# Kernel optimization log

Measured on AMD Instinct MI355X. Metric: run time of the kernel, lower is better.

## Reference

```python
import jax, jax.numpy as jnp
import numpy as np

B, IN_DIM, H, OUT_DIM, T = 2048, 1024, 2048, 1024, 10


def setup_inputs() -> dict:
    key = jax.random.key(0)
    ks = jax.random.split(key, 16)
    s = lambda d: 1.0 / np.sqrt(d)
    inp = {
        "x": jax.random.normal(ks[0], (B, IN_DIM), jnp.float32),
        "z0": jax.random.normal(ks[1], (B, H), jnp.float32),
        "noise": jax.random.normal(ks[2], (T, B, H), jnp.float32),
        # input_embed: Linear(IN,H) -> SiLU -> Linear(H,H)
        "w1_in": jax.random.normal(ks[3], (IN_DIM, H), jnp.float32) * s(IN_DIM),
        "b1_in": jnp.zeros((H,), jnp.float32),
        "w2_in": jax.random.normal(ks[4], (H, H), jnp.float32) * s(H),
        "b2_in": jnp.zeros((H,), jnp.float32),
        # T blocks: Linear(2H,H) -> SiLU -> Linear(H,H), stacked over T
        "wA": jax.random.normal(ks[5], (T, 2 * H, H), jnp.float32) * s(2 * H),
        "bA": jnp.zeros((T, H), jnp.float32),
        "wB": jax.random.normal(ks[6], (T, H, H), jnp.float32) * s(H),
        "bB": jnp.zeros((T, H), jnp.float32),
        # classifier Linear(H, OUT)
        "wC": jax.random.normal(ks[7], (H, OUT_DIM), jnp.float32) * s(H),
        "bC": jnp.zeros((OUT_DIM,), jnp.float32),
    }
    return inp


def _forward(x, z0, noise, w1_in, b1_in, w2_in, b2_in, wA, bA, wB, bB, wC, bC):
    # input embedding
    h = jax.nn.silu(x @ w1_in + b1_in)
    x_embed = h @ w2_in + b2_in  # (B, H)

    alpha = jnp.linspace(0.99, 0.9, T).astype(x.dtype)          # (T,)
    noise_scale = jnp.sqrt(1.0 - alpha)                          # (T,)

    def step(z, per_t):
        wA_t, bA_t, wB_t, bB_t, n_t, a_t, ns_t = per_t
        u = jax.nn.silu(jnp.concatenate([z, x_embed], axis=-1) @ wA_t + bA_t)
        u = u @ wB_t + bB_t
        z_next = a_t * u + (1.0 - a_t) * z + ns_t * n_t
        return z_next, None

    z_final, _ = jax.lax.scan(step, z0, (wA, bA, wB, bB, noise, alpha, noise_scale))
    return z_final @ wC + bC  # (B, OUT_DIM)


def reference(x, z0, noise, w1_in, b1_in, w2_in, b2_in, wA, bA, wB, bB, wC, bC):
    return _forward(x, z0, noise, w1_in, b1_in, w2_in, b2_in, wA, bA, wB, bB, wC, bC)
```

## Files before the change

### kernel.cpp

```cpp
#include <hip/hip_runtime.h>
#include <math.h>

typedef _Float16 f16;
typedef _Float16 f16x4 __attribute__((ext_vector_type(4)));
typedef _Float16 f16x8 __attribute__((ext_vector_type(8)));
typedef float f32x4 __attribute__((ext_vector_type(4)));
typedef float fvec4 __attribute__((ext_vector_type(4)));

#define EP_SILU 0
#define EP_LIN  1
#define EP_ZUP  2
#define EP_OUT  3
#define EP_ADDP 4

struct TDesc {
  const float* W;
  f16* WT;
  long long sW, sWT;
  int R, C, nMat;
};

__device__ __forceinline__ void gll16(const void* g, void* l) {
  __builtin_amdgcn_global_load_lds((__attribute__((address_space(1))) void*)g,
                                   (__attribute__((address_space(3))) void*)l,
                                   16, 0, 0);
}

__device__ __forceinline__ void stage_tile(const f16* __restrict__ g, int ld,
                                           f16* ldsTile, int tid, int wid) {
#pragma unroll
  for (int p = 0; p < 2; ++p) {
    int row = p * 64 + (tid >> 2);
    int col = (tid & 3) * 8;
    gll16(g + (size_t)row * ld + col, ldsTile + p * 2048 + wid * 512);
  }
}

__device__ __forceinline__ void stage8s(const f16* __restrict__ g, int ld,
                                        f16* ldsTile, int tid) {
  int row = tid >> 2;
  int q = (tid & 3) ^ ((tid >> 3) & 3);
  gll16(g + (size_t)row * ld + q * 8, ldsTile + tid * 8);
}

__device__ __forceinline__ void tpose_tile(const float* __restrict__ W,
                                           f16* __restrict__ WT, int R, int C,
                                           int r0, int c0, f16 (*t)[72],
                                           int tid) {
#pragma unroll
  for (int p = 0; p < 2; ++p) {
    int lin = p * 2048 + tid * 4;
    int r = lin >> 6, c4 = lin & 63;
    fvec4 v = *(const fvec4*)(W + (size_t)(r0 + r) * C + c0 + c4);
    t[c4 + 0][r] = (f16)v[0];
    t[c4 + 1][r] = (f16)v[1];
    t[c4 + 2][r] = (f16)v[2];
    t[c4 + 3][r] = (f16)v[3];
  }
  __syncthreads();
#pragma unroll
  for (int p = 0; p < 2; ++p) {
    int lin = p * 2048 + tid * 4;
    int c = lin >> 6, r4 = lin & 63;
    f16x4 h;
    h[0] = t[c][r4 + 0];
    h[1] = t[c][r4 + 1];
    h[2] = t[c][r4 + 2];
    h[3] = t[c][r4 + 3];
    *(f16x4*)(WT + (size_t)(c0 + c) * R + r0 + r4) = h;
  }
  __syncthreads();
}

__device__ void run_role(const TDesc d, int rid, int nr, f16 (*t)[72],
                         int tid) {
  if (d.nMat <= 0 || d.W == nullptr) return;
  int tR = d.R >> 6, tC = d.C >> 6;
  int tpm = tR * tC, tot = tpm * d.nMat;
  for (int i = rid; i < tot; i += nr) {
    int m = i / tpm, rem = i - m * tpm;
    int r0 = (rem % tR) << 6, c0 = (rem / tR) << 6;
    tpose_tile(d.W + (size_t)m * d.sW, d.WT + (size_t)m * d.sWT, d.R, d.C, r0,
               c0, t, tid);
  }
}

#define GEMM64_ITER(KP, VM, DO_STAGE)                                         \
  {                                                                           \
    asm volatile("s_waitcnt vmcnt(" #VM ")" ::: "memory");                    \
    __builtin_amdgcn_s_barrier();                                             \
    const int slot_ = (KP) & 1;                                               \
    const f16* LA_ = base + slot_ * 12288 + h * 2048;                         \
    const f16* LB_ = base + slot_ * 12288 + 4096 + h * 4096;                  \
    f16x8 a_[2], b_[4];                                                       \
    _Pragma("unroll") for (int m_ = 0; m_ < 2; ++m_) a_[m_] =                 \
        *(const f16x8*)(LA_ +                                                 \
                        ((wr * 32 + m_ * 16 + lr) * 32 + (kg ^ xq) * 8));     \
    _Pragma("unroll") for (int n_ = 0; n_ < 4; ++n_) b_[n_] =                 \
        *(const f16x8*)(LB_ +                                                 \
                        ((wc * 64 + n_ * 16 + lr) * 32 + (kg ^ xq) * 8));     \
    asm volatile("s_waitcnt lgkmcnt(0)" ::: "memory");                        \
    __builtin_amdgcn_s_barrier();                                             \
    if (DO_STAGE) stageAB((KP) + 2, slot_);                                   \
    _Pragma("unroll") for (int m_ = 0; m_ < 2; ++m_)                          \
        _Pragma("unroll") for (int n_ = 0; n_ < 4; ++n_) acc[m_][n_] =        \
            __builtin_amdgcn_mfma_f32_16x16x32_f16(a_[m_], b_[n_],            \
                                                   acc[m_][n_], 0, 0, 0);     \
  }

template <int EP>
__global__ void __launch_bounds__(512)
gemm64(const f16* __restrict__ A, int lda, const f16* __restrict__ BT,
       int ldb, int K, int N, int gx, int nbGemm,
       const float* __restrict__ bias, const f16* __restrict__ addP,
       f16* __restrict__ outH, float* __restrict__ outF,
       const f16* __restrict__ zOld, const float* __restrict__ noise,
       float aT, float nsT, TDesc dA, TDesc dB) {
  __shared__ __align__(16) char smem[49152];
  const int tid = threadIdx.x;
  const int bid = blockIdx.x;

  if (bid >= nbGemm) {
    int rid = bid - nbGemm, nr = (int)gridDim.x - nbGemm;
    f16(*t)[72] = reinterpret_cast<f16(*)[72]>(smem);
    run_role(dA, rid, nr, t, tid);
    run_role(dB, rid, nr, t, tid);
    return;
  }

  const int cpx = nbGemm >> 3;
  const int swz = (bid & 7) * cpx + (bid >> 3);
  const int by = swz / gx, bx = swz % gx;
  const int m0 = by * 64, n0 = bx * 128;

  const int lane = tid & 63, wid = tid >> 6;
  const int q = wid & 3, h = wid >> 2;
  const int wr = q >> 1, wc = q & 1;
  const int lr = lane & 15, kg = lane >> 4;
  const int xq = (lr >> 1) & 3;

  f16* base = (f16*)smem;
  f32x4 acc[2][4] = {};

  const int nkp = K >> 6;
  auto stageAB = [&](int kp, int slot) {
    int k0 = kp << 6;
    f16* s = base + slot * 12288;
    {
      int half = tid >> 8;
      int pos = tid & 255;
      int row = pos >> 2;
      int qq = (pos & 3) ^ ((pos >> 3) & 3);
      gll16(A + (size_t)(m0 + row) * lda + k0 + half * 32 + qq * 8,
            s + half * 2048 + pos * 8);
    }
    stage8s(BT + (size_t)n0 * ldb + k0, ldb, s + 4096, tid);
    stage8s(BT + (size_t)n0 * ldb + k0 + 32, ldb, s + 8192, tid);
  };

  stageAB(0, 0);
  stageAB(1, 1);
  int kp = 0;
  for (; kp < nkp - 1; ++kp) GEMM64_ITER(kp, 3, (kp + 2 < nkp));
  GEMM64_ITER(kp, 0, 0);

  float* red = (float*)smem;
  if (h == 1) {
#pragma unroll
    for (int m = 0; m < 2; ++m)
#pragma unroll
      for (int n = 0; n < 4; ++n) {
        int row = wr * 32 + m * 16 + kg * 4;
        int col = wc * 64 + n * 16 + lr;
        int rs = row ^ ((col & 7) << 2);
        *(f32x4*)&red[(size_t)col * 64 + rs] = acc[m][n];
      }
  }
  __syncthreads();
  if (h != 0) return;

  float bcol[4];
  if constexpr (EP != EP_ADDP) {
#pragma unroll
    for (int n = 0; n < 4; ++n) bcol[n] = bias[n0 + wc * 64 + n * 16 + lr];
  }

#pragma unroll
  for (int m = 0; m < 2; ++m) {
    int rowb = m0 + wr * 32 + m * 16 + kg * 4;
    int rowl = wr * 32 + m * 16 + kg * 4;
#pragma unroll
    for (int n = 0; n < 4; ++n) {
      int col = n0 + wc * 64 + n * 16 + lr;
      int coll = wc * 64 + n * 16 + lr;
      int rsl = rowl ^ ((coll & 7) << 2);
      f32x4 osum = acc[m][n] + *(const f32x4*)&red[(size_t)coll * 64 + rsl];
#pragma unroll
      for (int r = 0; r < 4; ++r) {
        size_t idx = (size_t)(rowb + r) * N + col;
        float v = osum[r];
        if constexpr (EP == EP_ADDP) v += (float)addP[idx];
        else v += bcol[n];
        if constexpr (EP == EP_SILU || EP == EP_ADDP) {
          v = v / (1.0f + __expf(-v));
          outH[idx] = (f16)v;
        } else if constexpr (EP == EP_LIN) {
          outH[idx] = (f16)v;
        } else if constexpr (EP == EP_OUT) {
          outF[idx] = v;
        } else {
          float zn = aT * v + (1.0f - aT) * (float)zOld[idx] + nsT * noise[idx];
          outH[idx] = (f16)zn;
        }
      }
    }
  }
}

#define GEMM8_ITER(KP, VM, DO_STAGE)                                          \
  {                                                                           \
    asm volatile("s_waitcnt vmcnt(" #VM ")" ::: "memory");                    \
    __builtin_amdgcn_s_barrier();                                             \
    const int slot_ = (KP) & 1;                                               \
    const f16* LA_ = base + slot_ * 16384 + h * 4096;                         \
    const f16* LB_ = base + slot_ * 16384 + 8192 + h * 4096;                  \
    f16x8 a_[4], b_[4];                                                       \
    _Pragma("unroll") for (int m_ = 0; m_ < 4; ++m_) a_[m_] =                 \
        *(const f16x8*)(LA_ +                                                 \
                        ((wr * 64 + m_ * 16 + lr) * 32 + (kg ^ xq) * 8));     \
    _Pragma("unroll") for (int n_ = 0; n_ < 4; ++n_) b_[n_] =                 \
        *(const f16x8*)(LB_ +                                                 \
                        ((wc * 64 + n_ * 16 + lr) * 32 + (kg ^ xq) * 8));     \
    asm volatile("s_waitcnt lgkmcnt(0)" ::: "memory");                        \
    __builtin_amdgcn_s_barrier();                                             \
    if (DO_STAGE) stageAB((KP) + 2, slot_);                                   \
    _Pragma("unroll") for (int m_ = 0; m_ < 4; ++m_)                          \
        _Pragma("unroll") for (int n_ = 0; n_ < 4; ++n_) acc[m_][n_] =        \
            __builtin_amdgcn_mfma_f32_16x16x32_f16(a_[m_], b_[n_],            \
                                                   acc[m_][n_], 0, 0, 0);     \
  }

template <int EP>
__global__ void __launch_bounds__(512)
gemm8(const f16* __restrict__ A, int lda, const f16* __restrict__ BT, int ldb,
      long long sBT, int K, int N, int gx, int nbGemm,
      const float* __restrict__ bias, long long sBias,
      f16* __restrict__ outH, long long sOut) {
  __shared__ __align__(16) char smem[65536];
  const int tid = threadIdx.x;
  const int bid = blockIdx.x;

  const int z = blockIdx.z;
  const f16* BTz = BT + (size_t)z * sBT;
  f16* outHz = outH + (size_t)z * sOut;

  const int cpx = nbGemm >> 3;
  const int swz = (bid & 7) * cpx + (bid >> 3);
  const int by = swz / gx, bx = swz % gx;
  const int m0 = by * 128, n0 = bx * 128;

  const int lane = tid & 63, wid = tid >> 6;
  const int q = wid & 3, h = wid >> 2;
  const int wr = q >> 1, wc = q & 1;
  const int lr = lane & 15, kg = lane >> 4;
  const int xq = (lr >> 1) & 3;

  f16* base = (f16*)smem;
  f32x4 acc[4][4] = {};

  const int nkp = K >> 6;
  auto stageAB = [&](int kp, int slot) {
    int k0 = kp << 6;
    f16* s = base + slot * 16384;
    stage8s(A + (size_t)m0 * lda + k0, lda, s, tid);
    stage8s(A + (size_t)m0 * lda + k0 + 32, lda, s + 4096, tid);
    stage8s(BTz + (size_t)n0 * ldb + k0, ldb, s + 8192, tid);
    stage8s(BTz + (size_t)n0 * ldb + k0 + 32, ldb, s + 12288, tid);
  };

  stageAB(0, 0);
  stageAB(1, 1);
  int kp = 0;
  for (; kp < nkp - 1; ++kp) GEMM8_ITER(kp, 4, (kp + 2 < nkp));
  GEMM8_ITER(kp, 0, 0);

  float* red = (float*)smem;
  if (h == 1) {
#pragma unroll
    for (int m = 0; m < 4; ++m)
#pragma unroll
      for (int n = 0; n < 4; ++n) {
        int row = wr * 64 + m * 16 + kg * 4;
        int col = wc * 64 + n * 16 + lr;
        int rs = row ^ ((col & 7) << 2);
        *(f32x4*)&red[(size_t)col * 128 + rs] = acc[m][n];
      }
  }
  __syncthreads();
  if (h != 0) return;

  float bcol[4];
  const float* biasz = bias + (size_t)z * sBias;
#pragma unroll
  for (int n = 0; n < 4; ++n) bcol[n] = biasz[n0 + wc * 64 + n * 16 + lr];

#pragma unroll
  for (int m = 0; m < 4; ++m) {
    int rowb = m0 + wr * 64 + m * 16 + kg * 4;
    int rowl = wr * 64 + m * 16 + kg * 4;
#pragma unroll
    for (int n = 0; n < 4; ++n) {
      int col = n0 + wc * 64 + n * 16 + lr;
      int coll = wc * 64 + n * 16 + lr;
      int rsl = rowl ^ ((coll & 7) << 2);
      f32x4 osum = acc[m][n] + *(const f32x4*)&red[(size_t)coll * 128 + rsl];
#pragma unroll
      for (int r = 0; r < 4; ++r) {
        size_t idx = (size_t)(rowb + r) * N + col;
        outHz[idx] = (f16)(osum[r] + bcol[n]);
      }
    }
  }
}

template <int EP>
__global__ void __launch_bounds__(256)
gemm_bt(const f16* __restrict__ A0, const f16* __restrict__ A1, int Ksplit,
        int lda, const f16* __restrict__ BT, int ldb, long long sBT, int K,
        int N, int gx, const float* __restrict__ bias, long long sBias,
        f16* __restrict__ outH, float* __restrict__ outF, long long sOut,
        const float* __restrict__ zOld, const float* __restrict__ noise,
        float aT, float nsT) {
  __shared__ __align__(16) f16 lds[2][2][128 * 32];
  const int tid = threadIdx.x;
  const int z = blockIdx.z;
  const f16* BTz = BT + (size_t)z * sBT;
  f16* outHz = outH ? outH + (size_t)z * sOut : nullptr;
  float* outFz = outF ? outF + (size_t)z * sOut : nullptr;

  const int lane = tid & 63, wid = tid >> 6;
  const int wr = wid >> 1, wc = wid & 1;
  const int lr = lane & 15, kg = lane >> 4;
  const int by = blockIdx.x / gx, bx = blockIdx.x - by * gx;
  const int m0 = by * 128, n0 = bx * 128;

  f32x4 acc[4][4] = {};
  const int nk = K >> 5;
  auto stageAB = [&](int kt, int buf) {
    int k0 = kt << 5;
    const f16* Abase = (k0 < Ksplit)
                           ? (A0 + (size_t)m0 * lda + k0)
                           : (A1 + (size_t)m0 * lda + (k0 - Ksplit));
    stage_tile(Abase, lda, &lds[buf][0][0], tid, wid);
    stage_tile(BTz + (size_t)n0 * ldb + k0, ldb, &lds[buf][1][0], tid, wid);
  };

  stageAB(0, 0);
  __syncthreads();
  int cur = 0;
  for (int kt = 0; kt < nk; ++kt) {
    if (kt + 1 < nk) stageAB(kt + 1, cur ^ 1);
    const f16* LA = &lds[cur][0][0];
    const f16* LB = &lds[cur][1][0];
    f16x8 a[4], b[4];
#pragma unroll
    for (int m = 0; m < 4; ++m)
      a[m] = *(const f16x8*)(LA + ((wr * 64 + m * 16 + lr) * 32 + kg * 8));
#pragma unroll
    for (int n = 0; n < 4; ++n)
      b[n] = *(const f16x8*)(LB + ((wc * 64 + n * 16 + lr) * 32 + kg * 8));
#pragma unroll
    for (int m = 0; m < 4; ++m)
#pragma unroll
      for (int n = 0; n < 4; ++n)
        acc[m][n] = __builtin_amdgcn_mfma_f32_16x16x32_f16(a[m], b[n],
                                                           acc[m][n], 0, 0, 0);
    __syncthreads();
    cur ^= 1;
  }

  float bcol[4];
  const float* biasz = bias + (size_t)z * sBias;
#pragma unroll
  for (int n = 0; n < 4; ++n) bcol[n] = biasz[n0 + wc * 64 + n * 16 + lr];

#pragma unroll
  for (int m = 0; m < 4; ++m) {
    int rowb = m0 + wr * 64 + m * 16 + kg * 4;
#pragma unroll
    for (int n = 0; n < 4; ++n) {
      int col = n0 + wc * 64 + n * 16 + lr;
#pragma unroll
      for (int r = 0; r < 4; ++r) {
        size_t idx = (size_t)(rowb + r) * N + col;
        float v = acc[m][n][r] + bcol[n];
        if constexpr (EP == EP_SILU) {
          v = v / (1.0f + __expf(-v));
          outHz[idx] = (f16)v;
        } else if constexpr (EP == EP_LIN) {
          outHz[idx] = (f16)v;
        } else if constexpr (EP == EP_OUT) {
          outFz[idx] = v;
        } else {
          float zn = aT * v + (1.0f - aT) * zOld[idx] + nsT * noise[idx];
          outFz[idx] = zn;
          outHz[idx] = (f16)zn;
        }
      }
    }
  }
}

__global__ void __launch_bounds__(512) tconv_role(TDesc d) {
  __shared__ __align__(16) f16 t[64][72];
  run_role(d, blockIdx.x, gridDim.x, t, threadIdx.x);
}

__global__ void __launch_bounds__(256)
cvt4(const float* __restrict__ in, f16* __restrict__ outp, int n4) {
  int i = blockIdx.x * 256 + threadIdx.x;
  if (i >= n4) return;
  fvec4 v = *(const fvec4*)(in + (size_t)i * 4);
  f16x4 h;
  h[0] = (f16)v[0];
  h[1] = (f16)v[1];
  h[2] = (f16)v[2];
  h[3] = (f16)v[3];
  *(f16x4*)(outp + (size_t)i * 4) = h;
}

__global__ void __launch_bounds__(256)
zinit4(const float* __restrict__ z0, float* __restrict__ z32,
       f16* __restrict__ z16, int n4) {
  int i = blockIdx.x * 256 + threadIdx.x;
  if (i >= n4) return;
  fvec4 v = *(const fvec4*)(z0 + (size_t)i * 4);
  *(fvec4*)(z32 + (size_t)i * 4) = v;
  f16x4 h;
  h[0] = (f16)v[0];
  h[1] = (f16)v[1];
  h[2] = (f16)v[2];
  h[3] = (f16)v[3];
  *(f16x4*)(z16 + (size_t)i * 4) = h;
}

extern "C" void kernel_launch(void* const* d_in, const int* in_sizes, int n_in,
                              void* d_out, int out_size, void* d_ws,
                              size_t ws_size, hipStream_t stream) {
  const int B = 2048, IN = 1024, H = 2048, OUT = 1024, T = 10;
  const float* x = (const float*)d_in[0];
  const float* z0 = (const float*)d_in[1];
  const float* noise = (const float*)d_in[2];
  const float* w1 = (const float*)d_in[3];
  const float* b1 = (const float*)d_in[4];
  const float* w2 = (const float*)d_in[5];
  const float* b2 = (const float*)d_in[6];
  const float* wA = (const float*)d_in[7];
  const float* bA = (const float*)d_in[8];
  const float* wB = (const float*)d_in[9];
  const float* bB = (const float*)d_in[10];
  const float* wC = (const float*)d_in[11];
  const float* bC = (const float*)d_in[12];
  float* out = (float*)d_out;

  char* ws = (char*)d_ws;
  size_t off = 0;
  auto alloc = [&](size_t bytes) {
    void* p = ws + off;
    off += (bytes + 255) & ~(size_t)255;
    return p;
  };
  TDesc none = {nullptr, nullptr, 0, 0, 0, 0, 0};

  const size_t FAST_NEED = 273000000ull;
  if (ws_size >= FAST_NEED) {
    f16* x16 = (f16*)alloc((size_t)B * IN * 2);
    f16* h16 = (f16*)alloc((size_t)B * H * 2);
    f16* xe16 = (f16*)alloc((size_t)B * H * 2);
    f16* z16 = (f16*)alloc((size_t)B * H * 2);
    f16* u16 = (f16*)alloc((size_t)B * H * 2);
    f16* p16 = (f16*)alloc((size_t)T * B * H * 2);
    f16* w1T = (f16*)alloc((size_t)IN * H * 2);
    f16* w2T = (f16*)alloc((size_t)H * H * 2);
    f16* wCT = (f16*)alloc((size_t)H * OUT * 2);
    f16* wAbotT = (f16*)alloc((size_t)T * H * H * 2);
    f16* wAtopT[2] = {(f16*)alloc((size_t)H * H * 2),
                      (f16*)alloc((size_t)H * H * 2)};
    f16* wBT2[2] = {(f16*)alloc((size_t)H * H * 2),
                    (f16*)alloc((size_t)H * H * 2)};

    cvt4<<<B * IN / 4 / 256, 256, 0, stream>>>(x, x16, B * IN / 4);
    cvt4<<<B * H / 4 / 256, 256, 0, stream>>>(z0, z16, B * H / 4);
    tconv_role<<<512, 512, 0, stream>>>(TDesc{w1, w1T, 0, 0, IN, H, 1});

    gemm64<EP_SILU><<<768, 512, 0, stream>>>(
        x16, IN, w1T, IN, IN, H, 16, 512, b1, nullptr, h16, nullptr, nullptr,
        nullptr, 0.f, 0.f, TDesc{w2, w2T, 0, 0, H, H, 1},
        TDesc{wA + (size_t)H * H, wAbotT, (long long)2 * H * H,
              (long long)H * H, H, H, 4});
    gemm64<EP_LIN><<<768, 512, 0, stream>>>(
        h16, H, w2T, H, H, H, 16, 512, b2, nullptr, xe16, nullptr, nullptr,
        nullptr, 0.f, 0.f, TDesc{wC, wCT, 0, 0, H, OUT, 1},
        TDesc{wA + (size_t)H * H + (size_t)4 * 2 * H * H,
              wAbotT + (size_t)4 * H * H, (long long)2 * H * H,
              (long long)H * H, H, H, 6});
    tconv_role<<<512, 512, 0, stream>>>(TDesc{wA, wAtopT[0], 0, 0, H, H, 1});

    gemm8<EP_LIN><<<dim3(256, 1, T), 512, 0, stream>>>(
        xe16, H, wAbotT, H, (long long)H * H, H, H, 16, 256, bA, H, p16,
        (long long)B * H);

    for (int t = 0; t < T; ++t) {
      float alpha = (float)(0.99 - 0.01 * (double)t);
      float ns = sqrtf(1.0f - alpha);
      gemm64<EP_ADDP><<<576, 512, 0, stream>>>(
          z16, H, wAtopT[t & 1], H, H, H, 16, 512, nullptr,
          p16 + (size_t)t * B * H, u16, nullptr, nullptr, nullptr, 0.f, 0.f,
          TDesc{wB + (size_t)t * H * H, wBT2[t & 1], 0, 0, H, H, 1}, none);
      TDesc nextA = (t < T - 1)
                        ? TDesc{wA + (size_t)(t + 1) * 2 * H * H,
                                wAtopT[(t + 1) & 1], 0, 0, H, H, 1}
                        : none;
      gemm64<EP_ZUP><<<576, 512, 0, stream>>>(
          u16, H, wBT2[t & 1], H, H, H, 16, 512, bB + (size_t)t * H, nullptr,
          z16, nullptr, z16, noise + (size_t)t * B * H, alpha, ns, nextA,
          none);
    }
    gemm64<EP_OUT><<<256, 512, 0, stream>>>(
        z16, H, wCT, H, H, OUT, 8, 256, bC, nullptr, nullptr, out, nullptr,
        nullptr, 0.f, 0.f, none, none);
  } else {
    f16* x16 = (f16*)alloc((size_t)B * IN * 2);
    f16* h16 = (f16*)alloc((size_t)B * H * 2);
    f16* xe16 = (f16*)alloc((size_t)B * H * 2);
    f16* z16 = (f16*)alloc((size_t)B * H * 2);
    f16* u16 = (f16*)alloc((size_t)B * H * 2);
    float* z32 = (float*)alloc((size_t)B * H * 4);
    f16* w1T = (f16*)alloc((size_t)IN * H * 2);
    f16* w2T = (f16*)alloc((size_t)H * H * 2);
    f16* wCT = (f16*)alloc((size_t)H * OUT * 2);
    f16* wAT = (f16*)alloc((size_t)2 * H * H * 2);
    f16* wBT = (f16*)alloc((size_t)H * H * 2);

    cvt4<<<B * IN / 4 / 256, 256, 0, stream>>>(x, x16, B * IN / 4);
    zinit4<<<B * H / 4 / 256, 256, 0, stream>>>(z0, z32, z16, B * H / 4);
    tconv_role<<<512, 512, 0, stream>>>(TDesc{w1, w1T, 0, 0, IN, H, 1});
    tconv_role<<<1024, 512, 0, stream>>>(TDesc{w2, w2T, 0, 0, H, H, 1});
    tconv_role<<<512, 512, 0, stream>>>(TDesc{wC, wCT, 0, 0, H, OUT, 1});

    gemm_bt<EP_SILU><<<dim3(256, 1, 1), 256, 0, stream>>>(
        x16, x16, IN, IN, w1T, IN, 0, IN, H, 16, b1, 0, h16, nullptr, 0,
        nullptr, nullptr, 0.f, 0.f);
    gemm_bt<EP_LIN><<<dim3(256, 1, 1), 256, 0, stream>>>(
        h16, h16, H, H, w2T, H, 0, H, H, 16, b2, 0, xe16, nullptr, 0, nullptr,
        nullptr, 0.f, 0.f);

    for (int t = 0; t < T; ++t) {
      float alpha = (float)(0.99 - 0.01 * (double)t);
      float ns = sqrtf(1.0f - alpha);
      tconv_role<<<1024, 512, 0, stream>>>(
          TDesc{wA + (size_t)t * 2 * H * H, wAT, 0, 0, 2 * H, H, 1});
      gemm_bt<EP_SILU><<<dim3(256, 1, 1), 256, 0, stream>>>(
          z16, xe16, H, H, wAT, 2 * H, 0, 2 * H, H, 16, bA + (size_t)t * H, 0,
          u16, nullptr, 0, nullptr, nullptr, 0.f, 0.f);
      tconv_role<<<1024, 512, 0, stream>>>(
          TDesc{wB + (size_t)t * H * H, wBT, 0, 0, H, H, 1});
      gemm_bt<EP_ZUP><<<dim3(256, 1, 1), 256, 0, stream>>>(
          u16, u16, H, H, wBT, H, 0, H, H, 16, bB + (size_t)t * H, 0, z16,
          z32, 0, z32, noise + (size_t)t * B * H, alpha, ns);
    }
    gemm_bt<EP_OUT><<<dim3(128, 1, 1), 256, 0, stream>>>(
        z16, z16, H, H, wCT, H, 0, H, OUT, 8, bC, 0, nullptr, out, 0, nullptr,
        nullptr, 0.f, 0.f);
  }
}
```

Measured before the change: 1.177 ms.

## Replace 64x128 GEMM tiles with 128x128 split-K GEMM and atomic-flag reduction

Replaces the 64-row tile GEMM used for the embedding, per-step, and classifier matmuls with a 128x128 tile kernel that splits K in half across two blocks. Each block writes fp32 partials to a global scratch buffer, and the second block to arrive, detected with an atomic counter per tile, reduces the partials and runs the fused epilogue. The larger tiles increase data reuse per block while split-K keeps the block count unchanged. The cost is extra global scratch traffic, threadfence synchronisation, a flags memset, and more workspace. The transpose-role split between the two embedding GEMMs is also rebalanced.

```diff
diff --git a/kernel.cpp b/kernel.cpp
--- a/kernel.cpp
+++ b/kernel.cpp
@@ -82,138 +82,6 @@
     int r0 = (rem % tR) << 6, c0 = (rem / tR) << 6;
     tpose_tile(d.W + (size_t)m * d.sW, d.WT + (size_t)m * d.sWT, d.R, d.C, r0,
                c0, t, tid);
-  }
-}
-
-#define GEMM64_ITER(KP, VM, DO_STAGE)                                         \
-  {                                                                           \
-    asm volatile("s_waitcnt vmcnt(" #VM ")" ::: "memory");                    \
-    __builtin_amdgcn_s_barrier();                                             \
-    const int slot_ = (KP) & 1;                                               \
-    const f16* LA_ = base + slot_ * 12288 + h * 2048;                         \
-    const f16* LB_ = base + slot_ * 12288 + 4096 + h * 4096;                  \
-    f16x8 a_[2], b_[4];                                                       \
-    _Pragma("unroll") for (int m_ = 0; m_ < 2; ++m_) a_[m_] =                 \
-        *(const f16x8*)(LA_ +                                                 \
-                        ((wr * 32 + m_ * 16 + lr) * 32 + (kg ^ xq) * 8));     \
-    _Pragma("unroll") for (int n_ = 0; n_ < 4; ++n_) b_[n_] =                 \
-        *(const f16x8*)(LB_ +                                                 \
-                        ((wc * 64 + n_ * 16 + lr) * 32 + (kg ^ xq) * 8));     \
-    asm volatile("s_waitcnt lgkmcnt(0)" ::: "memory");                        \
-    __builtin_amdgcn_s_barrier();                                             \
-    if (DO_STAGE) stageAB((KP) + 2, slot_);                                   \
-    _Pragma("unroll") for (int m_ = 0; m_ < 2; ++m_)                          \
-        _Pragma("unroll") for (int n_ = 0; n_ < 4; ++n_) acc[m_][n_] =        \
-            __builtin_amdgcn_mfma_f32_16x16x32_f16(a_[m_], b_[n_],            \
-                                                   acc[m_][n_], 0, 0, 0);     \
-  }
-
-template <int EP>
-__global__ void __launch_bounds__(512)
-gemm64(const f16* __restrict__ A, int lda, const f16* __restrict__ BT,
-       int ldb, int K, int N, int gx, int nbGemm,
-       const float* __restrict__ bias, const f16* __restrict__ addP,
-       f16* __restrict__ outH, float* __restrict__ outF,
-       const f16* __restrict__ zOld, const float* __restrict__ noise,
-       float aT, float nsT, TDesc dA, TDesc dB) {
-  __shared__ __align__(16) char smem[49152];
-  const int tid = threadIdx.x;
-  const int bid = blockIdx.x;
-
-  if (bid >= nbGemm) {
-    int rid = bid - nbGemm, nr = (int)gridDim.x - nbGemm;
-    f16(*t)[72] = reinterpret_cast<f16(*)[72]>(smem);
-    run_role(dA, rid, nr, t, tid);
-    run_role(dB, rid, nr, t, tid);
-    return;
-  }
-
-  const int cpx = nbGemm >> 3;
-  const int swz = (bid & 7) * cpx + (bid >> 3);
-  const int by = swz / gx, bx = swz % gx;
-  const int m0 = by * 64, n0 = bx * 128;
-
-  const int lane = tid & 63, wid = tid >> 6;
-  const int q = wid & 3, h = wid >> 2;
-  const int wr = q >> 1, wc = q & 1;
-  const int lr = lane & 15, kg = lane >> 4;
-  const int xq = (lr >> 1) & 3;
-
-  f16* base = (f16*)smem;
-  f32x4 acc[2][4] = {};
-
-  const int nkp = K >> 6;
-  auto stageAB = [&](int kp, int slot) {
-    int k0 = kp << 6;
-    f16* s = base + slot * 12288;
-    {
-      int half = tid >> 8;
-      int pos = tid & 255;
-      int row = pos >> 2;
-      int qq = (pos & 3) ^ ((pos >> 3) & 3);
-      gll16(A + (size_t)(m0 + row) * lda + k0 + half * 32 + qq * 8,
-            s + half * 2048 + pos * 8);
-    }
-    stage8s(BT + (size_t)n0 * ldb + k0, ldb, s + 4096, tid);
-    stage8s(BT + (size_t)n0 * ldb + k0 + 32, ldb, s + 8192, tid);
-  };
-
-  stageAB(0, 0);
-  stageAB(1, 1);
-  int kp = 0;
-  for (; kp < nkp - 1; ++kp) GEMM64_ITER(kp, 3, (kp + 2 < nkp));
-  GEMM64_ITER(kp, 0, 0);
-
-  float* red = (float*)smem;
-  if (h == 1) {
-#pragma unroll
-    for (int m = 0; m < 2; ++m)
-#pragma unroll
-      for (int n = 0; n < 4; ++n) {
-        int row = wr * 32 + m * 16 + kg * 4;
-        int col = wc * 64 + n * 16 + lr;
-        int rs = row ^ ((col & 7) << 2);
-        *(f32x4*)&red[(size_t)col * 64 + rs] = acc[m][n];
-      }
-  }
-  __syncthreads();
-  if (h != 0) return;
-
-  float bcol[4];
-  if constexpr (EP != EP_ADDP) {
-#pragma unroll
-    for (int n = 0; n < 4; ++n) bcol[n] = bias[n0 + wc * 64 + n * 16 + lr];
-  }
-
-#pragma unroll
-  for (int m = 0; m < 2; ++m) {
-    int rowb = m0 + wr * 32 + m * 16 + kg * 4;
-    int rowl = wr * 32 + m * 16 + kg * 4;
-#pragma unroll
-    for (int n = 0; n < 4; ++n) {
-      int col = n0 + wc * 64 + n * 16 + lr;
-      int coll = wc * 64 + n * 16 + lr;
-      int rsl = rowl ^ ((coll & 7) << 2);
-      f32x4 osum = acc[m][n] + *(const f32x4*)&red[(size_t)coll * 64 + rsl];
-#pragma unroll
-      for (int r = 0; r < 4; ++r) {
-        size_t idx = (size_t)(rowb + r) * N + col;
-        float v = osum[r];
-        if constexpr (EP == EP_ADDP) v += (float)addP[idx];
-        else v += bcol[n];
-        if constexpr (EP == EP_SILU || EP == EP_ADDP) {
-          v = v / (1.0f + __expf(-v));
-          outH[idx] = (f16)v;
-        } else if constexpr (EP == EP_LIN) {
-          outH[idx] = (f16)v;
-        } else if constexpr (EP == EP_OUT) {
-          outF[idx] = v;
-        } else {
-          float zn = aT * v + (1.0f - aT) * (float)zOld[idx] + nsT * noise[idx];
-          outH[idx] = (f16)zn;
-        }
-      }
-    }
   }
 }
 
@@ -244,12 +112,10 @@
 __global__ void __launch_bounds__(512)
 gemm8(const f16* __restrict__ A, int lda, const f16* __restrict__ BT, int ldb,
       long long sBT, int K, int N, int gx, int nbGemm,
-      const float* __restrict__ bias, long long sBias,
-      f16* __restrict__ outH, long long sOut) {
+      const float* __restrict__ bias, long long sBias, f16* __restrict__ outH,
+      long long sOut) {
   __shared__ __align__(16) char smem[65536];
-  const int tid = threadIdx.x;
-  const int bid = blockIdx.x;
-
+  const int tid = threadIdx.x, bid = blockIdx.x;
   const int z = blockIdx.z;
   const f16* BTz = BT + (size_t)z * sBT;
   f16* outHz = outH + (size_t)z * sOut;
@@ -318,6 +184,134 @@
       for (int r = 0; r < 4; ++r) {
         size_t idx = (size_t)(rowb + r) * N + col;
         outHz[idx] = (f16)(osum[r] + bcol[n]);
+      }
+    }
+  }
+}
+
+template <int EP>
+__global__ void __launch_bounds__(512)
+gemmsk(const f16* __restrict__ A, int lda, const f16* __restrict__ BT,
+       int ldb, int K, int N, int gx, int nt, const float* __restrict__ bias,
+       const f16* __restrict__ addP, f16* __restrict__ outH,
+       float* __restrict__ outF, const f16* __restrict__ zOld,
+       const float* __restrict__ noise, float aT, float nsT,
+       float* __restrict__ scratch, unsigned* __restrict__ flags, TDesc dA,
+       TDesc dB) {
+  __shared__ __align__(16) char smem[65536];
+  __shared__ unsigned who;
+  const int tid = threadIdx.x, bid = blockIdx.x;
+
+  if (bid >= 2 * nt) {
+    int rid = bid - 2 * nt, nr = (int)gridDim.x - 2 * nt;
+    f16(*t)[72] = reinterpret_cast<f16(*)[72]>(smem);
+    run_role(dA, rid, nr, t, tid);
+    run_role(dB, rid, nr, t, tid);
+    return;
+  }
+
+  const int kh = bid >= nt;
+  const int p = bid - kh * nt;
+  const int cpx = nt >> 3;
+  const int swz = (p & 7) * cpx + (p >> 3);
+  const int by = swz / gx, bx = swz % gx;
+  const int m0 = by * 128, n0 = bx * 128;
+
+  const int lane = tid & 63, wid = tid >> 6;
+  const int q = wid & 3, h = wid >> 2;
+  const int wr = q >> 1, wc = q & 1;
+  const int lr = lane & 15, kg = lane >> 4;
+  const int xq = (lr >> 1) & 3;
+
+  f16* base = (f16*)smem;
+  f32x4 acc[4][4] = {};
+
+  const int Khalf = K >> 1;
+  const int kOff = kh * Khalf;
+  const int nkp = Khalf >> 6;
+  auto stageAB = [&](int kp, int slot) {
+    int k0 = kOff + (kp << 6);
+    f16* s = base + slot * 16384;
+    stage8s(A + (size_t)m0 * lda + k0, lda, s, tid);
+    stage8s(A + (size_t)m0 * lda + k0 + 32, lda, s + 4096, tid);
+    stage8s(BT + (size_t)n0 * ldb + k0, ldb, s + 8192, tid);
+    stage8s(BT + (size_t)n0 * ldb + k0 + 32, ldb, s + 12288, tid);
+  };
+
+  stageAB(0, 0);
+  stageAB(1, 1);
+  int kp = 0;
+  for (; kp < nkp - 1; ++kp) GEMM8_ITER(kp, 4, (kp + 2 < nkp));
+  GEMM8_ITER(kp, 0, 0);
+
+  float* red = (float*)smem;
+  if (h == 1) {
+#pragma unroll
+    for (int m = 0; m < 4; ++m)
+#pragma unroll
+      for (int n = 0; n < 4; ++n) {
+        int row = wr * 64 + m * 16 + kg * 4;
+        int col = wc * 64 + n * 16 + lr;
+        int rs = row ^ ((col & 7) << 2);
+        *(f32x4*)&red[(size_t)col * 128 + rs] = acc[m][n];
+      }
+  }
+  __syncthreads();
+  float* scr = scratch + (size_t)p * 32768;
+  if (h == 0) {
+#pragma unroll
+    for (int m = 0; m < 4; ++m) {
+      int rowl = wr * 64 + m * 16 + kg * 4;
+#pragma unroll
+      for (int n = 0; n < 4; ++n) {
+        int coll = wc * 64 + n * 16 + lr;
+        int rsl = rowl ^ ((coll & 7) << 2);
+        acc[m][n] += *(const f32x4*)&red[(size_t)coll * 128 + rsl];
+        *(f32x4*)&scr[(size_t)kh * 16384 + (m * 4 + n) * 1024 + tid * 4] =
+            acc[m][n];
+      }
+    }
+  }
+  __syncthreads();
+  if (tid == 0) {
+    __threadfence();
+    who = atomicAdd(&flags[p], 1u);
+  }
+  __syncthreads();
+  if (who != 1u || h != 0) return;
+
+  __threadfence();
+  const float* ps = scr + (size_t)(kh ^ 1) * 16384;
+  float bcol[4];
+  if constexpr (EP != EP_ADDP) {
+#pragma unroll
+    for (int n = 0; n < 4; ++n) bcol[n] = bias[n0 + wc * 64 + n * 16 + lr];
+  }
+#pragma unroll
+  for (int m = 0; m < 4; ++m) {
+    int rowb = m0 + wr * 64 + m * 16 + kg * 4;
+#pragma unroll
+    for (int n = 0; n < 4; ++n) {
+      int col = n0 + wc * 64 + n * 16 + lr;
+      f32x4 osum =
+          acc[m][n] + *(const f32x4*)&ps[(m * 4 + n) * 1024 + tid * 4];
+#pragma unroll
+      for (int r = 0; r < 4; ++r) {
+        size_t idx = (size_t)(rowb + r) * N + col;
+        float v = osum[r];
+        if constexpr (EP == EP_ADDP) v += (float)addP[idx];
+        else v += bcol[n];
+        if constexpr (EP == EP_SILU || EP == EP_ADDP) {
+          v = v / (1.0f + __expf(-v));
+          outH[idx] = (f16)v;
+        } else if constexpr (EP == EP_LIN) {
+          outH[idx] = (f16)v;
+        } else if constexpr (EP == EP_OUT) {
+          outF[idx] = v;
+        } else {
+          float zn = aT * v + (1.0f - aT) * (float)zOld[idx] + nsT * noise[idx];
+          outH[idx] = (f16)zn;
+        }
       }
     }
   }
@@ -472,8 +466,10 @@
   };
   TDesc none = {nullptr, nullptr, 0, 0, 0, 0, 0};
 
-  const size_t FAST_NEED = 273000000ull;
+  const size_t FAST_NEED = 312000000ull;
   if (ws_size >= FAST_NEED) {
+    unsigned* flags = (unsigned*)alloc(24 * 256 * 4);
+    float* scratch = (float*)alloc((size_t)256 * 32768 * 4);
     f16* x16 = (f16*)alloc((size_t)B * IN * 2);
     f16* h16 = (f16*)alloc((size_t)B * H * 2);
     f16* xe16 = (f16*)alloc((size_t)B * H * 2);
@@ -489,21 +485,24 @@
     f16* wBT2[2] = {(f16*)alloc((size_t)H * H * 2),
                     (f16*)alloc((size_t)H * H * 2)};
 
+    hipMemsetAsync(flags, 0, 24 * 256 * 4, stream);
     cvt4<<<B * IN / 4 / 256, 256, 0, stream>>>(x, x16, B * IN / 4);
     cvt4<<<B * H / 4 / 256, 256, 0, stream>>>(z0, z16, B * H / 4);
     tconv_role<<<512, 512, 0, stream>>>(TDesc{w1, w1T, 0, 0, IN, H, 1});
 
-    gemm64<EP_SILU><<<768, 512, 0, stream>>>(
-        x16, IN, w1T, IN, IN, H, 16, 512, b1, nullptr, h16, nullptr, nullptr,
-        nullptr, 0.f, 0.f, TDesc{w2, w2T, 0, 0, H, H, 1},
+    gemmsk<EP_SILU><<<768, 512, 0, stream>>>(
+        x16, IN, w1T, IN, IN, H, 16, 256, b1, nullptr, h16, nullptr, nullptr,
+        nullptr, 0.f, 0.f, scratch, flags + 0 * 256,
+        TDesc{w2, w2T, 0, 0, H, H, 1},
         TDesc{wA + (size_t)H * H, wAbotT, (long long)2 * H * H,
-              (long long)H * H, H, H, 4});
-    gemm64<EP_LIN><<<768, 512, 0, stream>>>(
-        h16, H, w2T, H, H, H, 16, 512, b2, nullptr, xe16, nullptr, nullptr,
-        nullptr, 0.f, 0.f, TDesc{wC, wCT, 0, 0, H, OUT, 1},
-        TDesc{wA + (size_t)H * H + (size_t)4 * 2 * H * H,
-              wAbotT + (size_t)4 * H * H, (long long)2 * H * H,
-              (long long)H * H, H, H, 6});
+              (long long)H * H, H, H, 5});
+    gemmsk<EP_LIN><<<768, 512, 0, stream>>>(
+        h16, H, w2T, H, H, H, 16, 256, b2, nullptr, xe16, nullptr, nullptr,
+        nullptr, 0.f, 0.f, scratch, flags + 1 * 256,
+        TDesc{wC, wCT, 0, 0, H, OUT, 1},
+        TDesc{wA + (size_t)H * H + (size_t)5 * 2 * H * H,
+              wAbotT + (size_t)5 * H * H, (long long)2 * H * H,
+              (long long)H * H, H, H, 5});
     tconv_role<<<512, 512, 0, stream>>>(TDesc{wA, wAtopT[0], 0, 0, H, H, 1});
 
     gemm8<EP_LIN><<<dim3(256, 1, T), 512, 0, stream>>>(
@@ -513,22 +512,23 @@
     for (int t = 0; t < T; ++t) {
       float alpha = (float)(0.99 - 0.01 * (double)t);
       float ns = sqrtf(1.0f - alpha);
-      gemm64<EP_ADDP><<<576, 512, 0, stream>>>(
-          z16, H, wAtopT[t & 1], H, H, H, 16, 512, nullptr,
+      gemmsk<EP_ADDP><<<576, 512, 0, stream>>>(
+          z16, H, wAtopT[t & 1], H, H, H, 16, 256, nullptr,
           p16 + (size_t)t * B * H, u16, nullptr, nullptr, nullptr, 0.f, 0.f,
+          scratch, flags + (2 + 2 * t) * 256,
           TDesc{wB + (size_t)t * H * H, wBT2[t & 1], 0, 0, H, H, 1}, none);
       TDesc nextA = (t < T - 1)
                         ? TDesc{wA + (size_t)(t + 1) * 2 * H * H,
                                 wAtopT[(t + 1) & 1], 0, 0, H, H, 1}
                         : none;
-      gemm64<EP_ZUP><<<576, 512, 0, stream>>>(
-          u16, H, wBT2[t & 1], H, H, H, 16, 512, bB + (size_t)t * H, nullptr,
-          z16, nullptr, z16, noise + (size_t)t * B * H, alpha, ns, nextA,
-          none);
+      gemmsk<EP_ZUP><<<576, 512, 0, stream>>>(
+          u16, H, wBT2[t & 1], H, H, H, 16, 256, bB + (size_t)t * H, nullptr,
+          z16, nullptr, z16, noise + (size_t)t * B * H, alpha, ns, scratch,
+          flags + (3 + 2 * t) * 256, nextA, none);
     }
-    gemm64<EP_OUT><<<256, 512, 0, stream>>>(
-        z16, H, wCT, H, H, OUT, 8, 256, bC, nullptr, nullptr, out, nullptr,
-        nullptr, 0.f, 0.f, none, none);
+    gemmsk<EP_OUT><<<256, 512, 0, stream>>>(
+        z16, H, wCT, H, H, OUT, 8, 128, bC, nullptr, nullptr, out, nullptr,
+        nullptr, 0.f, 0.f, scratch, flags + 22 * 256, none, none);
   } else {
     f16* x16 = (f16*)alloc((size_t)B * IN * 2);
     f16* h16 = (f16*)alloc((size_t)B * H * 2);
```

Measured after the change: 2.515 ms. 114% more time.
